# Optimization experiments

Hardware: AMD Instinct MI355X
Metric: run time of the kernel (lower is better)

Reference implementation:

```python
import jax, jax.numpy as jnp
import numpy as np

B, T, C, H = 2, 2048, 1024, 16
D = C // H  # head dim = 64


def setup_inputs() -> dict:
    key = jax.random.key(0)
    ks = jax.random.split(key, 5)
    s = 0.02
    return {
        "x": jax.random.normal(ks[0], (B, T, C), dtype=jnp.float32),
        "W_attn": jax.random.normal(ks[1], (C, 3 * C), dtype=jnp.float32) * s,
        "b_attn": jax.random.normal(ks[2], (3 * C,), dtype=jnp.float32) * s,
        "W_proj": jax.random.normal(ks[3], (C, C), dtype=jnp.float32) * s,
        "b_proj": jax.random.normal(ks[4], (C,), dtype=jnp.float32) * s,
    }


def reference(x, W_attn, b_attn, W_proj, b_proj):
    Bb, Tt, Cc = x.shape
    kqv = x @ W_attn + b_attn                     # [B,T,3C]
    q, k, v = jnp.split(kqv, 3, axis=2)           # each [B,T,C]
    # reshape to heads: [B,H,T,D]
    q = q.reshape(Bb, Tt, H, D).transpose(0, 2, 1, 3)
    k = k.reshape(Bb, Tt, H, D).transpose(0, 2, 1, 3)
    v = v.reshape(Bb, Tt, H, D).transpose(0, 2, 1, 3)
    scale = 1.0 / jnp.sqrt(jnp.float32(D))
    att = jnp.einsum('bhqd,bhkd->bhqk', q, k) * scale  # [B,H,T,T]
    causal = jnp.tril(jnp.ones((Tt, Tt), dtype=bool))
    att = jnp.where(causal[None, None], att, -jnp.inf)
    att = jax.nn.softmax(att, axis=-1)
    y = jnp.einsum('bhqk,bhkd->bhqd', att, v)      # [B,H,T,D]
    y = y.transpose(0, 2, 1, 3).reshape(Bb, Tt, Cc)
    return y @ W_proj + b_proj
```

## Files before the change

### kernel.cpp

```cpp
#include <hip/hip_runtime.h>
#include <hip/hip_bf16.h>
#include <math.h>

typedef __attribute__((ext_vector_type(4))) float f32x4;
typedef __attribute__((ext_vector_type(8))) short short8;
typedef __attribute__((ext_vector_type(4))) short short4v;

__device__ __forceinline__ short f2bf(float f) {
    union { __hip_bfloat16 h; short s; } u;
    u.h = __float2bfloat16(f);
    return u.s;
}

__global__ __launch_bounds__(256) void cvt_bf16(const float* __restrict__ in,
                                                short* __restrict__ out, int n) {
    int i = (blockIdx.x * 256 + threadIdx.x) * 8;
    if (i >= n) return;
    float4 a = *reinterpret_cast<const float4*>(in + i);
    float4 b = *reinterpret_cast<const float4*>(in + i + 4);
    short8 o;
    o[0] = f2bf(a.x); o[1] = f2bf(a.y); o[2] = f2bf(a.z); o[3] = f2bf(a.w);
    o[4] = f2bf(b.x); o[5] = f2bf(b.y); o[6] = f2bf(b.z); o[7] = f2bf(b.w);
    *reinterpret_cast<short8*>(out + i) = o;
}

__global__ __launch_bounds__(256) void transpose_w(const float* __restrict__ W,
                                                   short* __restrict__ Wt,
                                                   int K, int N) {
    __shared__ float tile[64][68];
    const int k0 = blockIdx.x * 64;
    const int n0 = blockIdx.y * 64;
    const int tid = threadIdx.x;
    #pragma unroll
    for (int i = 0; i < 4; ++i) {
        int c = tid + i * 256;
        int r = c >> 4;
        int col4 = (c & 15) * 4;
        float4 v = *reinterpret_cast<const float4*>(W + (size_t)(k0 + r) * N + n0 + col4);
        tile[r][col4 + 0] = v.x; tile[r][col4 + 1] = v.y;
        tile[r][col4 + 2] = v.z; tile[r][col4 + 3] = v.w;
    }
    __syncthreads();
    #pragma unroll
    for (int i = 0; i < 4; ++i) {
        int c = tid + i * 256;
        int r2 = c >> 4;
        int col4 = (c & 15) * 4;
        short4v o;
        #pragma unroll
        for (int j = 0; j < 4; ++j) o[j] = f2bf(tile[col4 + j][r2]);
        *reinterpret_cast<short4v*>(Wt + (size_t)(n0 + r2) * K + k0 + col4) = o;
    }
}

template<int MODE>
__global__ __launch_bounds__(256) void gemm_bt(const short* __restrict__ A,
                                               const short* __restrict__ Bt,
                                               const float* __restrict__ bias,
                                               void* __restrict__ C,
                                               short* __restrict__ vt,
                                               int M, int N, int K) {
    constexpr int BM = 128, BN = 128, BK = 64, LDP = BK + 8;
    __shared__ short As[BM * LDP];
    __shared__ short Bs[BN * LDP];
    const int tid = threadIdx.x;
    const int lane = tid & 63, wave = tid >> 6;
    const int bm = blockIdx.x * BM, bn = blockIdx.y * BN;
    const int wr = (wave >> 1) * 64, wc = (wave & 1) * 64;
    const int g = lane >> 4, l15 = lane & 15;

    f32x4 acc[4][4] = {};

    for (int k0 = 0; k0 < K; k0 += BK) {
        __syncthreads();
        #pragma unroll
        for (int i = 0; i < 4; ++i) {
            int c = tid + i * 256;
            int r = c >> 3;
            int col = (c & 7) * 8;
            *reinterpret_cast<short8*>(&As[r * LDP + col]) =
                *reinterpret_cast<const short8*>(A + (size_t)(bm + r) * K + k0 + col);
            *reinterpret_cast<short8*>(&Bs[r * LDP + col]) =
                *reinterpret_cast<const short8*>(Bt + (size_t)(bn + r) * K + k0 + col);
        }
        __syncthreads();
        #pragma unroll
        for (int kk = 0; kk < 2; ++kk) {
            short8 af[4], bfr[4];
            #pragma unroll
            for (int m = 0; m < 4; ++m)
                af[m] = *reinterpret_cast<const short8*>(&As[(wr + m * 16 + l15) * LDP + kk * 32 + g * 8]);
            #pragma unroll
            for (int n = 0; n < 4; ++n)
                bfr[n] = *reinterpret_cast<const short8*>(&Bs[(wc + n * 16 + l15) * LDP + kk * 32 + g * 8]);
            #pragma unroll
            for (int m = 0; m < 4; ++m)
                #pragma unroll
                for (int n = 0; n < 4; ++n)
                    acc[m][n] = __builtin_amdgcn_mfma_f32_16x16x32_bf16(af[m], bfr[n], acc[m][n], 0, 0, 0);
        }
    }

    #pragma unroll
    for (int m = 0; m < 4; ++m)
        #pragma unroll
        for (int n = 0; n < 4; ++n) {
            int gc = bn + wc + n * 16 + l15;
            float bv = bias[gc];
            int gr0 = bm + wr + m * 16 + g * 4;
            if (MODE == 0) {
                #pragma unroll
                for (int r = 0; r < 4; ++r)
                    reinterpret_cast<float*>(C)[(size_t)(gr0 + r) * N + gc] = acc[m][n][r] + bv;
            } else {
                if (gc < 2048) {
                    float sc = (gc < 1024) ? 0.125f : 1.0f;
                    short* qkp = reinterpret_cast<short*>(C);
                    #pragma unroll
                    for (int r = 0; r < 4; ++r)
                        qkp[(size_t)(gr0 + r) * 2048 + gc] = f2bf((acc[m][n][r] + bv) * sc);
                } else {
                    int cv = gc - 2048;
                    int bb = gr0 >> 11;
                    int t0 = gr0 & 2047;
                    short4v o;
                    #pragma unroll
                    for (int r = 0; r < 4; ++r) o[r] = f2bf(acc[m][n][r] + bv);
                    *reinterpret_cast<short4v*>(&vt[((size_t)(bb << 10) + cv) * 2048 + t0]) = o;
                }
            }
        }
}

__global__ __launch_bounds__(256) void attn_kernel(const short* __restrict__ qk,
                                                   const short* __restrict__ vt,
                                                   short* __restrict__ yatt) {
    constexpr int T = 2048;
    constexpr int LDK = 72;
    __shared__ short Ks[64 * LDK];
    __shared__ short Vs[64 * LDK];
    __shared__ short Ps[4][16 * LDK];

    const int tid = threadIdx.x;
    const int lane = tid & 63, wave = tid >> 6;
    const int g = lane >> 4, l15 = lane & 15;

    const int i = blockIdx.x;
    const int x = i & 7;
    const int u = i >> 3;
    const int g2 = u >> 5;
    const int v = u & 31;
    const int qt = (g2 & 1) ? v : 31 - v;
    const int grp = x * 4 + g2;
    const int h = grp & 15, b = grp >> 4;

    const int qs = qt * 64;
    const int q0w = qs + wave * 16;

    const size_t baseQ = (size_t)b * T * 2048 + (size_t)h * 64;
    const size_t baseK = baseQ + 1024;
    const size_t vbase = ((size_t)b * 1024 + (size_t)h * 64) * 2048;

    short8 qf[2];
    #pragma unroll
    for (int kk = 0; kk < 2; ++kk)
        qf[kk] = *reinterpret_cast<const short8*>(
            qk + baseQ + (size_t)(q0w + l15) * 2048 + kk * 32 + g * 8);

    f32x4 oacc[4] = {};
    float mst[4], lst[4];
    #pragma unroll
    for (int r = 0; r < 4; ++r) { mst[r] = -INFINITY; lst[r] = 0.f; }

    for (int j = 0; j <= qt; ++j) {
        const int kb = j * 64;
        __syncthreads();
        #pragma unroll
        for (int it = 0; it < 2; ++it) {
            int c = tid + it * 256;
            int r = c >> 3;
            int col = (c & 7) * 8;
            *reinterpret_cast<short8*>(&Ks[r * LDK + col]) =
                *reinterpret_cast<const short8*>(qk + baseK + (size_t)(kb + r) * 2048 + col);
            *reinterpret_cast<short8*>(&Vs[r * LDK + col]) =
                *reinterpret_cast<const short8*>(vt + vbase + (size_t)r * 2048 + kb + col);
        }
        __syncthreads();

        const bool diag = (j == qt);
        const int nmax = diag ? (wave | 1) : 3;

        f32x4 sacc[4] = {};
        __builtin_amdgcn_s_setprio(1);
        #pragma unroll
        for (int kk = 0; kk < 2; ++kk) {
            #pragma unroll
            for (int n = 0; n < 4; ++n) {
                if (n > nmax) break;
                short8 bfr = *reinterpret_cast<const short8*>(&Ks[(n * 16 + l15) * LDK + kk * 32 + g * 8]);
                sacc[n] = __builtin_amdgcn_mfma_f32_16x16x32_bf16(qf[kk], bfr, sacc[n], 0, 0, 0);
            }
        }
        __builtin_amdgcn_s_setprio(0);

        if (diag) {
            #pragma unroll
            for (int n = 0; n < 4; ++n) {
                if (n > nmax) break;
                #pragma unroll
                for (int r = 0; r < 4; ++r) {
                    int row = q0w + g * 4 + r;
                    int col = kb + n * 16 + l15;
                    if (col > row) sacc[n][r] = -INFINITY;
                }
            }
        }

        #pragma unroll
        for (int r = 0; r < 4; ++r) {
            float rm = sacc[0][r];
            #pragma unroll
            for (int n = 1; n < 4; ++n) {
                if (n > nmax) break;
                rm = fmaxf(rm, sacc[n][r]);
            }
            #pragma unroll
            for (int w = 1; w < 16; w <<= 1) rm = fmaxf(rm, __shfl_xor(rm, w));
            float mn = fmaxf(mst[r], rm);
            float corr = __expf(mst[r] - mn);
            mst[r] = mn;
            float ls = 0.f;
            #pragma unroll
            for (int n = 0; n < 4; ++n) {
                if (n > nmax) break;
                float p = __expf(sacc[n][r] - mn);
                ls += p;
                Ps[wave][(g * 4 + r) * LDK + n * 16 + l15] = f2bf(p);
            }
            #pragma unroll
            for (int w = 1; w < 16; w <<= 1) ls += __shfl_xor(ls, w);
            lst[r] = lst[r] * corr + ls;
            #pragma unroll
            for (int nd = 0; nd < 4; ++nd) oacc[nd][r] *= corr;
        }

        const int kkmax = diag ? (wave >> 1) : 1;
        __builtin_amdgcn_s_setprio(1);
        #pragma unroll
        for (int kk = 0; kk < 2; ++kk) {
            if (kk > kkmax) break;
            short8 pa = *reinterpret_cast<const short8*>(&Ps[wave][l15 * LDK + kk * 32 + g * 8]);
            #pragma unroll
            for (int nd = 0; nd < 4; ++nd) {
                short8 vb = *reinterpret_cast<const short8*>(&Vs[(nd * 16 + l15) * LDK + kk * 32 + g * 8]);
                oacc[nd] = __builtin_amdgcn_mfma_f32_16x16x32_bf16(pa, vb, oacc[nd], 0, 0, 0);
            }
        }
        __builtin_amdgcn_s_setprio(0);
    }

    #pragma unroll
    for (int r = 0; r < 4; ++r) {
        float rl = 1.0f / lst[r];
        int row = q0w + g * 4 + r;
        #pragma unroll
        for (int nd = 0; nd < 4; ++nd) {
            int col = nd * 16 + l15;
            yatt[((size_t)b * T + row) * 1024 + h * 64 + col] = f2bf(oacc[nd][r] * rl);
        }
    }
}

extern "C" void kernel_launch(void* const* d_in, const int* in_sizes, int n_in,
                              void* d_out, int out_size, void* d_ws, size_t ws_size,
                              hipStream_t stream) {
    constexpr int B = 2, T = 2048, C = 1024;
    constexpr int M = B * T;
    constexpr int N1 = 3 * C;
    constexpr int K = C;

    const float* x      = (const float*)d_in[0];
    const float* W_attn = (const float*)d_in[1];
    const float* b_attn = (const float*)d_in[2];
    const float* W_proj = (const float*)d_in[3];
    const float* b_proj = (const float*)d_in[4];
    float* out = (float*)d_out;

    char* ws = (char*)d_ws;
    short* x_bf    = (short*)(ws);
    short* Wt_attn = (short*)(ws + 8388608);
    short* Wt_proj = (short*)(ws + 14680064);
    short* qk      = (short*)(ws + 16777216);
    short* vt      = (short*)(ws + 33554432);
    short* yatt    = (short*)(ws + 41943040);

    cvt_bf16<<<dim3(M * K / (256 * 8)), 256, 0, stream>>>(x, x_bf, M * K);
    transpose_w<<<dim3(K / 64, N1 / 64), 256, 0, stream>>>(W_attn, Wt_attn, K, N1);
    transpose_w<<<dim3(K / 64, C / 64), 256, 0, stream>>>(W_proj, Wt_proj, K, C);

    gemm_bt<1><<<dim3(M / 128, N1 / 128), 256, 0, stream>>>(x_bf, Wt_attn, b_attn, qk, vt, M, N1, K);
    attn_kernel<<<dim3(1024), 256, 0, stream>>>(qk, vt, yatt);
    gemm_bt<0><<<dim3(M / 128, C / 128), 256, 0, stream>>>(yatt, Wt_proj, b_proj, out, nullptr, M, C, C);
}
```

Baseline: 181.6 us.

## Restructure attention into single-wave blocks loading K/V fragments directly from global

The attention kernel now runs one 64-thread wave per block, each handling 32 query rows (two 16-row MFMA tiles). K and V fragments are read straight from global memory into registers, so there is no shared-memory staging and no block barriers. The row sum is computed with an MFMA against a vector of ones instead of shuffle reductions. The diagonal tile is specialised through template parameters. This removes syncthreads and LDS traffic and doubles K/V reuse per wave, at the cost of more global loads per wave and more registers.

```diff
diff --git a/kernel.cpp b/kernel.cpp
--- a/kernel.cpp
+++ b/kernel.cpp
@@ -10,6 +10,10 @@
     union { __hip_bfloat16 h; short s; } u;
     u.h = __float2bfloat16(f);
     return u.s;
+}
+
+__device__ __forceinline__ f32x4 mfma16(short8 a, short8 b, f32x4 c) {
+    return __builtin_amdgcn_mfma_f32_16x16x32_bf16(a, b, c, 0, 0, 0);
 }
 
 __global__ __launch_bounds__(256) void cvt_bf16(const float* __restrict__ in,
@@ -97,7 +101,7 @@
             for (int m = 0; m < 4; ++m)
                 #pragma unroll
                 for (int n = 0; n < 4; ++n)
-                    acc[m][n] = __builtin_amdgcn_mfma_f32_16x16x32_bf16(af[m], bfr[n], acc[m][n], 0, 0, 0);
+                    acc[m][n] = mfma16(af[m], bfr[n], acc[m][n]);
         }
     }
 
@@ -132,143 +136,161 @@
         }
 }
 
-__global__ __launch_bounds__(256) void attn_kernel(const short* __restrict__ qk,
-                                                   const short* __restrict__ vt,
-                                                   short* __restrict__ yatt) {
-    constexpr int T = 2048;
-    constexpr int LDK = 72;
-    __shared__ short Ks[64 * LDK];
-    __shared__ short Vs[64 * LDK];
-    __shared__ short Ps[4][16 * LDK];
-
-    const int tid = threadIdx.x;
-    const int lane = tid & 63, wave = tid >> 6;
-    const int g = lane >> 4, l15 = lane & 15;
-
-    const int i = blockIdx.x;
-    const int x = i & 7;
-    const int u = i >> 3;
-    const int g2 = u >> 5;
-    const int v = u & 31;
-    const int qt = (g2 & 1) ? v : 31 - v;
-    const int grp = x * 4 + g2;
-    const int h = grp & 15, b = grp >> 4;
-
-    const int qs = qt * 64;
-    const int q0w = qs + wave * 16;
-
-    const size_t baseQ = (size_t)b * T * 2048 + (size_t)h * 64;
-    const size_t baseK = baseQ + 1024;
-    const size_t vbase = ((size_t)b * 1024 + (size_t)h * 64) * 2048;
-
-    short8 qf[2];
+
+template<int NMAX, int KKMAX, bool MASK>
+__device__ __forceinline__ void tile_step(const short* __restrict__ Kl,
+                                          const short* __restrict__ Vl,
+                                          short* Ps, int l15, int g,
+                                          const short8 (&qf)[2][2],
+                                          f32x4 (&oacc)[2][4],
+                                          f32x4 (&lacc)[2],
+                                          float (&mst)[2][4],
+                                          int rowbase, int colbase,
+                                          short8 ones) {
+    f32x4 sacc[2][NMAX + 1];
+    #pragma unroll
+    for (int m = 0; m < 2; ++m)
+        #pragma unroll
+        for (int n = 0; n <= NMAX; ++n) sacc[m][n] = f32x4{0.f, 0.f, 0.f, 0.f};
+    __builtin_amdgcn_s_setprio(1);
     #pragma unroll
     for (int kk = 0; kk < 2; ++kk)
-        qf[kk] = *reinterpret_cast<const short8*>(
-            qk + baseQ + (size_t)(q0w + l15) * 2048 + kk * 32 + g * 8);
-
-    f32x4 oacc[4] = {};
-    float mst[4], lst[4];
-    #pragma unroll
-    for (int r = 0; r < 4; ++r) { mst[r] = -INFINITY; lst[r] = 0.f; }
-
-    for (int j = 0; j <= qt; ++j) {
-        const int kb = j * 64;
-        __syncthreads();
-        #pragma unroll
-        for (int it = 0; it < 2; ++it) {
-            int c = tid + it * 256;
-            int r = c >> 3;
-            int col = (c & 7) * 8;
-            *reinterpret_cast<short8*>(&Ks[r * LDK + col]) =
-                *reinterpret_cast<const short8*>(qk + baseK + (size_t)(kb + r) * 2048 + col);
-            *reinterpret_cast<short8*>(&Vs[r * LDK + col]) =
-                *reinterpret_cast<const short8*>(vt + vbase + (size_t)r * 2048 + kb + col);
-        }
-        __syncthreads();
-
-        const bool diag = (j == qt);
-        const int nmax = diag ? (wave | 1) : 3;
-
-        f32x4 sacc[4] = {};
-        __builtin_amdgcn_s_setprio(1);
-        #pragma unroll
-        for (int kk = 0; kk < 2; ++kk) {
-            #pragma unroll
-            for (int n = 0; n < 4; ++n) {
-                if (n > nmax) break;
-                short8 bfr = *reinterpret_cast<const short8*>(&Ks[(n * 16 + l15) * LDK + kk * 32 + g * 8]);
-                sacc[n] = __builtin_amdgcn_mfma_f32_16x16x32_bf16(qf[kk], bfr, sacc[n], 0, 0, 0);
-            }
-        }
-        __builtin_amdgcn_s_setprio(0);
-
-        if (diag) {
-            #pragma unroll
-            for (int n = 0; n < 4; ++n) {
-                if (n > nmax) break;
+        #pragma unroll
+        for (int n = 0; n <= NMAX; ++n) {
+            short8 kf = *reinterpret_cast<const short8*>(Kl + (size_t)n * 16 * 2048 + kk * 32);
+            sacc[0][n] = mfma16(qf[0][kk], kf, sacc[0][n]);
+            sacc[1][n] = mfma16(qf[1][kk], kf, sacc[1][n]);
+        }
+    __builtin_amdgcn_s_setprio(0);
+
+    short8 vf[KKMAX + 1][4];
+    #pragma unroll
+    for (int kk = 0; kk <= KKMAX; ++kk)
+        #pragma unroll
+        for (int nd = 0; nd < 4; ++nd)
+            vf[kk][nd] = *reinterpret_cast<const short8*>(Vl + (size_t)nd * 16 * 2048 + kk * 32);
+
+    if (MASK) {
+        #pragma unroll
+        for (int m = 0; m < 2; ++m)
+            #pragma unroll
+            for (int n = 0; n <= NMAX; ++n)
                 #pragma unroll
                 for (int r = 0; r < 4; ++r) {
-                    int row = q0w + g * 4 + r;
-                    int col = kb + n * 16 + l15;
-                    if (col > row) sacc[n][r] = -INFINITY;
+                    int row = rowbase + m * 16 + r;
+                    int col = colbase + n * 16;
+                    if (col > row) sacc[m][n][r] = -INFINITY;
                 }
+    }
+
+    #pragma unroll
+    for (int m = 0; m < 2; ++m)
+        #pragma unroll
+        for (int r = 0; r < 4; ++r) {
+            float rm = sacc[m][0][r];
+            #pragma unroll
+            for (int n = 1; n <= NMAX; ++n) rm = fmaxf(rm, sacc[m][n][r]);
+            #pragma unroll
+            for (int w = 1; w < 16; w <<= 1) rm = fmaxf(rm, __shfl_xor(rm, w));
+            float mn = fmaxf(mst[m][r], rm);
+            float corr = __expf(mst[m][r] - mn);
+            mst[m][r] = mn;
+            #pragma unroll
+            for (int n = 0; n <= NMAX; ++n) {
+                float p = __expf(sacc[m][n][r] - mn);
+                Ps[(g * 4 + m * 16 + r) * 72 + n * 16 + l15] = f2bf(p);
             }
-        }
-
+            lacc[m][r] *= corr;
+            #pragma unroll
+            for (int nd = 0; nd < 4; ++nd) oacc[m][nd][r] *= corr;
+        }
+
+    __builtin_amdgcn_s_setprio(1);
+    #pragma unroll
+    for (int kk = 0; kk <= KKMAX; ++kk) {
+        short8 pa0 = *reinterpret_cast<const short8*>(&Ps[l15 * 72 + kk * 32 + g * 8]);
+        short8 pa1 = *reinterpret_cast<const short8*>(&Ps[(16 + l15) * 72 + kk * 32 + g * 8]);
+        #pragma unroll
+        for (int nd = 0; nd < 4; ++nd) {
+            oacc[0][nd] = mfma16(pa0, vf[kk][nd], oacc[0][nd]);
+            oacc[1][nd] = mfma16(pa1, vf[kk][nd], oacc[1][nd]);
+        }
+        lacc[0] = mfma16(pa0, ones, lacc[0]);
+        lacc[1] = mfma16(pa1, ones, lacc[1]);
+    }
+    __builtin_amdgcn_s_setprio(0);
+}
+
+__global__ __launch_bounds__(64) void attn_kernel(const short* __restrict__ qk,
+                                                  const short* __restrict__ vt,
+                                                  short* __restrict__ yatt) {
+    constexpr int T = 2048;
+    __shared__ short Ps[32 * 72];
+
+    const int lane = threadIdx.x & 63;
+    const int g = lane >> 4, l15 = lane & 15;
+
+    const int bid = blockIdx.x;
+    const int xcd = bid & 7;
+    const int idx = bid >> 3;
+    const int grp = xcd * 4 + (idx >> 6);
+    const int h = grp & 15, b = grp >> 4;
+    const int qt = 63 - (idx & 63);
+    const int qs = qt * 32;
+
+    const size_t baseQ = (size_t)b * T * 2048 + (size_t)h * 64;
+    const short* Kl = qk + baseQ + 1024 + (size_t)l15 * 2048 + g * 8;
+    const short* Vl = vt + ((size_t)b * 1024 + (size_t)h * 64) * 2048 + (size_t)l15 * 2048 + g * 8;
+
+    short8 ones;
+    #pragma unroll
+    for (int i = 0; i < 8; ++i) ones[i] = (short)0x3F80;
+
+    short8 qf[2][2];
+    #pragma unroll
+    for (int m = 0; m < 2; ++m)
+        #pragma unroll
+        for (int kk = 0; kk < 2; ++kk)
+            qf[m][kk] = *reinterpret_cast<const short8*>(
+                qk + baseQ + (size_t)(qs + m * 16 + l15) * 2048 + kk * 32 + g * 8);
+
+    f32x4 oacc[2][4] = {};
+    f32x4 lacc[2] = {};
+    float mst[2][4];
+    #pragma unroll
+    for (int m = 0; m < 2; ++m)
+        #pragma unroll
+        for (int r = 0; r < 4; ++r) mst[m][r] = -INFINITY;
+
+    const int rowbase = qs + g * 4;
+    int colbase = l15;
+    const int jd = qt >> 1;
+
+    const short* Klj = Kl;
+    const short* Vlj = Vl;
+    for (int j = 0; j < jd; ++j) {
+        tile_step<3, 1, false>(Klj, Vlj, Ps, l15, g, qf, oacc, lacc, mst, rowbase, colbase, ones);
+        Klj += 64 * 2048;
+        Vlj += 64;
+        colbase += 64;
+    }
+    if (qt & 1)
+        tile_step<3, 1, true>(Klj, Vlj, Ps, l15, g, qf, oacc, lacc, mst, rowbase, colbase, ones);
+    else
+        tile_step<1, 0, true>(Klj, Vlj, Ps, l15, g, qf, oacc, lacc, mst, rowbase, colbase, ones);
+
+    #pragma unroll
+    for (int m = 0; m < 2; ++m)
         #pragma unroll
         for (int r = 0; r < 4; ++r) {
-            float rm = sacc[0][r];
-            #pragma unroll
-            for (int n = 1; n < 4; ++n) {
-                if (n > nmax) break;
-                rm = fmaxf(rm, sacc[n][r]);
+            float rl = 1.0f / lacc[m][r];
+            int row = qs + m * 16 + g * 4 + r;
+            #pragma unroll
+            for (int nd = 0; nd < 4; ++nd) {
+                int col = nd * 16 + l15;
+                yatt[((size_t)b * T + row) * 1024 + h * 64 + col] = f2bf(oacc[m][nd][r] * rl);
             }
-            #pragma unroll
-            for (int w = 1; w < 16; w <<= 1) rm = fmaxf(rm, __shfl_xor(rm, w));
-            float mn = fmaxf(mst[r], rm);
-            float corr = __expf(mst[r] - mn);
-            mst[r] = mn;
-            float ls = 0.f;
-            #pragma unroll
-            for (int n = 0; n < 4; ++n) {
-                if (n > nmax) break;
-                float p = __expf(sacc[n][r] - mn);
-                ls += p;
-                Ps[wave][(g * 4 + r) * LDK + n * 16 + l15] = f2bf(p);
-            }
-            #pragma unroll
-            for (int w = 1; w < 16; w <<= 1) ls += __shfl_xor(ls, w);
-            lst[r] = lst[r] * corr + ls;
-            #pragma unroll
-            for (int nd = 0; nd < 4; ++nd) oacc[nd][r] *= corr;
-        }
-
-        const int kkmax = diag ? (wave >> 1) : 1;
-        __builtin_amdgcn_s_setprio(1);
-        #pragma unroll
-        for (int kk = 0; kk < 2; ++kk) {
-            if (kk > kkmax) break;
-            short8 pa = *reinterpret_cast<const short8*>(&Ps[wave][l15 * LDK + kk * 32 + g * 8]);
-            #pragma unroll
-            for (int nd = 0; nd < 4; ++nd) {
-                short8 vb = *reinterpret_cast<const short8*>(&Vs[(nd * 16 + l15) * LDK + kk * 32 + g * 8]);
-                oacc[nd] = __builtin_amdgcn_mfma_f32_16x16x32_bf16(pa, vb, oacc[nd], 0, 0, 0);
-            }
-        }
-        __builtin_amdgcn_s_setprio(0);
-    }
-
-    #pragma unroll
-    for (int r = 0; r < 4; ++r) {
-        float rl = 1.0f / lst[r];
-        int row = q0w + g * 4 + r;
-        #pragma unroll
-        for (int nd = 0; nd < 4; ++nd) {
-            int col = nd * 16 + l15;
-            yatt[((size_t)b * T + row) * 1024 + h * 64 + col] = f2bf(oacc[nd][r] * rl);
-        }
-    }
+        }
 }
 
 extern "C" void kernel_launch(void* const* d_in, const int* in_sizes, int n_in,
@@ -299,6 +321,6 @@
     transpose_w<<<dim3(K / 64, C / 64), 256, 0, stream>>>(W_proj, Wt_proj, K, C);
 
     gemm_bt<1><<<dim3(M / 128, N1 / 128), 256, 0, stream>>>(x_bf, Wt_attn, b_attn, qk, vt, M, N1, K);
-    attn_kernel<<<dim3(1024), 256, 0, stream>>>(qk, vt, yatt);
+    attn_kernel<<<dim3(2048), 64, 0, stream>>>(qk, vt, yatt);
     gemm_bt<0><<<dim3(M / 128, C / 128), 256, 0, stream>>>(yatt, Wt_proj, b_proj, out, nullptr, M, C, C);
 }
```

After: 184.4 us. No clear change (+1.5%).
